# Kernel tuning notes

Hardware: AMD Instinct MI355X
Metric: run time of the kernel (lower is better)

## Reference

```python
import jax, jax.numpy as jnp
import numpy as np
from jax import lax

DIM = 256
NUM_HEADS = 8
HEAD_DIM = DIM // NUM_HEADS
SCALE = HEAD_DIM ** -0.5


def _avg_pool(x, k, p):
    # torch AvgPool2d(kernel=k, stride=1, padding=p) with count_include_pad=True
    s = lax.reduce_window(x, 0.0, lax.add,
                          window_dimensions=(1, 1, k, k),
                          window_strides=(1, 1, 1, 1),
                          padding=((0, 0), (0, 0), (p, p), (p, p)))
    return s / (k * k)


def setup_inputs() -> dict:
    key = jax.random.key(0)
    ks = jax.random.split(key, 7)
    x = jax.random.normal(ks[0], (2, DIM, 48, 48), dtype=jnp.float32)
    q_w = jax.random.normal(ks[1], (DIM, DIM), dtype=jnp.float32) * (DIM ** -0.5)
    q_b = jax.random.normal(ks[2], (DIM,), dtype=jnp.float32) * 0.02
    kv_w = jax.random.normal(ks[3], (2 * DIM, DIM), dtype=jnp.float32) * (DIM ** -0.5)
    kv_b = jax.random.normal(ks[4], (2 * DIM,), dtype=jnp.float32) * 0.02
    proj_w = jax.random.normal(ks[5], (DIM, DIM), dtype=jnp.float32) * (DIM ** -0.5)
    proj_b = jax.random.normal(ks[6], (DIM,), dtype=jnp.float32) * 0.02
    return {"x": x, "q_w": q_w, "q_b": q_b, "kv_w": kv_w, "kv_b": kv_b,
            "proj_w": proj_w, "proj_b": proj_b}


def reference(x, q_w, q_b, kv_w, kv_b, proj_w, proj_b):
    B, C, H, W = x.shape
    h, d, N = NUM_HEADS, HEAD_DIM, H * W

    # q = 1x1 conv -> [B, h, N, d]
    q = jnp.einsum('oc,bchw->bohw', q_w, x) + q_b[None, :, None, None]
    q = q.reshape(B, h, d, N).transpose(0, 1, 3, 2)

    # kv is a linear 1x1 conv, so (kv(x)+kv(p1)+kv(p2)+kv(p3))/4 == kv(mean of inputs)
    x_avg = (x + _avg_pool(x, 3, 1) + _avg_pool(x, 5, 2) + _avg_pool(x, 7, 3)) / 4.0
    kv = jnp.einsum('oc,bchw->bohw', kv_w, x_avg) + kv_b[None, :, None, None]
    kv = kv.reshape(B, 2, h, d, N).transpose(1, 0, 2, 4, 3)  # [2, B, h, N, d]
    k, v = kv[0], kv[1]

    attn = jnp.einsum('bhnd,bhmd->bhnm', q, k) * SCALE  # [B, h, N, N]
    attn = jax.nn.softmax(attn, axis=-1)
    y = jnp.einsum('bhnm,bhmd->bhnd', attn, v)  # [B, h, N, d]
    # faithful to torch: transpose(1,2) then flat reshape to [B, C, H, W]
    y = y.transpose(0, 2, 1, 3).reshape(B, C, H, W)

    out = jnp.einsum('oc,bchw->bohw', proj_w, y) + proj_b[None, :, None, None]
    return out
```

## Files before the change

kernel.cpp:

```cpp
#include <hip/hip_runtime.h>
#include <hip/hip_bf16.h>
#include <cstdint>

#define DIMC  256
#define NH    8
#define HD    32
#define NPIX  2304
#define BATCH 2
#define NSPLIT 6
#define KPS   384
#define KT    32
#define NT    (KPS / KT)

typedef short s16x8 __attribute__((ext_vector_type(8)));
typedef short s16x4 __attribute__((ext_vector_type(4)));
typedef float f32x4 __attribute__((ext_vector_type(4)));

#define MFMA32(A,B,C) __builtin_amdgcn_mfma_f32_16x16x32_bf16(A,B,C,0,0,0)

__device__ inline uint32_t rnau(float x) { return __float_as_uint(x) + 0x8000u; }
__device__ inline uint32_t pk2(uint32_t l_, uint32_t h_) {
  return __builtin_amdgcn_perm(h_, l_, 0x07060302u);
}

__global__ __launch_bounds__(256) void pool_kernel(const float* __restrict__ x,
                                                   float* __restrict__ xavg) {
  const int plane = blockIdx.x;
  const float* xp = x + (size_t)plane * NPIX;
  __shared__ float sx[NPIX];
  __shared__ float h3[NPIX], h5[NPIX], h7[NPIX];
  const int t = threadIdx.x;
#pragma unroll
  for (int r = 0; r < 9; ++r) sx[r * 256 + t] = xp[r * 256 + t];
  __syncthreads();
#pragma unroll
  for (int r = 0; r < 9; ++r) {
    int p = r * 256 + t;
    int i = p / 48, j = p - i * 48;
    float a3 = 0.f, a5 = 0.f, a7 = 0.f;
#pragma unroll
    for (int dj = -3; dj <= 3; ++dj) {
      int jj = j + dj;
      if (jj < 0 || jj >= 48) continue;
      float v = sx[i * 48 + jj];
      a7 += v;
      if (dj >= -2 && dj <= 2) a5 += v;
      if (dj >= -1 && dj <= 1) a3 += v;
    }
    h3[p] = a3; h5[p] = a5; h7[p] = a7;
  }
  __syncthreads();
#pragma unroll
  for (int r = 0; r < 9; ++r) {
    int p = r * 256 + t;
    int i = p / 48, j = p - i * 48;
    float b3 = 0.f, b5 = 0.f, b7 = 0.f;
#pragma unroll
    for (int di = -3; di <= 3; ++di) {
      int ii = i + di;
      if (ii < 0 || ii >= 48) continue;
      int q = ii * 48 + j;
      b7 += h7[q];
      if (di >= -2 && di <= 2) b5 += h5[q];
      if (di >= -1 && di <= 1) b3 += h3[q];
    }
    xavg[(size_t)plane * NPIX + p] =
        0.25f * (sx[p] + b3 * (1.f / 9.f) + b5 * (1.f / 25.f) + b7 * (1.f / 49.f));
  }
}

__global__ __launch_bounds__(256) void conv_all(
    const float* __restrict__ x, const float* __restrict__ xavg,
    const float* __restrict__ qw, const float* __restrict__ kvw,
    const float* __restrict__ pw_,
    short* __restrict__ Xh, short* __restrict__ Ah,
    short* __restrict__ Wth) {
  const int bx = blockIdx.x;
  const int t = threadIdx.x;
  if (bx < 576) {
    const float* src = (bx < 288) ? x : xavg;
    short* dhi = (bx < 288) ? Xh : Ah;
    const int bb = (bx < 288) ? bx : bx - 288;
    const int n0 = (bb % 36) * 64, c0 = ((bb / 36) & 3) * 64, b = bb / 144;
    __shared__ __align__(16) float T[64][68];
    {
      const int c = t >> 2, n4 = (t & 3) * 16;
      const float* sp = src + ((size_t)b * DIMC + c0 + c) * NPIX + n0 + n4;
#pragma unroll
      for (int i2 = 0; i2 < 4; ++i2)
        *(f32x4*)&T[c][n4 + i2 * 4] = *(const f32x4*)(sp + i2 * 4);
    }
    __syncthreads();
    {
      const int n = t >> 2, c4 = (t & 3) * 16;
      float v[16];
#pragma unroll
      for (int i = 0; i < 16; ++i) v[i] = T[c4 + i][n];
      uint32_t a[16];
#pragma unroll
      for (int i = 0; i < 16; ++i) a[i] = rnau(v[i]);
      union { s16x8 s; uint32_t u[4]; } H0, H1;
#pragma unroll
      for (int j = 0; j < 4; ++j) {
        H0.u[j] = pk2(a[2 * j], a[2 * j + 1]);
        H1.u[j] = pk2(a[8 + 2 * j], a[8 + 2 * j + 1]);
      }
      const size_t off = ((size_t)b * NPIX + n0 + n) * DIMC + c0 + c4;
      *(s16x8*)(dhi + off) = H0.s; *(s16x8*)(dhi + off + 8) = H1.s;
    }
  } else {
    const int idx = ((bx - 576) * 256 + t) * 8;
    const float* s;
    int off;
    if (idx < 65536)       { s = qw;  off = idx; }
    else if (idx < 196608) { s = kvw; off = idx - 65536; }
    else                   { s = pw_; off = idx - 196608; }
    f32x4 x0 = *(const f32x4*)(s + off);
    f32x4 x1 = *(const f32x4*)(s + off + 4);
    float v[8] = {x0[0], x0[1], x0[2], x0[3], x1[0], x1[1], x1[2], x1[3]};
    uint32_t a[8];
#pragma unroll
    for (int i = 0; i < 8; ++i) a[i] = rnau(v[i]);
    union { s16x8 s; uint32_t u[4]; } H;
#pragma unroll
    for (int j = 0; j < 4; ++j) H.u[j] = pk2(a[2 * j], a[2 * j + 1]);
    *(s16x8*)(Wth + idx) = H.s;
  }
}

__global__ __launch_bounds__(128) void gemm_qkv_hi(
    const short* __restrict__ Wth,
    const float* __restrict__ q_b, const float* __restrict__ kv_b,
    const short* __restrict__ Xh, const short* __restrict__ Ah,
    short* __restrict__ Qhi, short* __restrict__ Khi, short* __restrict__ Vhi,
    float qscale) {
  __shared__ __align__(16) float Cl[32][68];
  const int by = blockIdx.y;
  const bool isQ = (by < 8);
  const int o0 = isQ ? by * 32 : (by - 8) * 32;
  const short* Wh = isQ ? Wth : Wth + 65536;
  const float* bias = isQ ? q_b : kv_b;
  const short* Inh = isQ ? Xh : Ah;
  const float scale = isQ ? qscale : 1.0f;
  short* d1 = isQ ? Qhi : Khi;
  const int n0 = blockIdx.x * 64;
  const int b  = blockIdx.z;

  const int tid = threadIdx.x;
  const int wave = tid >> 6, lane = tid & 63;
  const int g = lane >> 4, q = lane & 15;

  const short* wph = Wh + ((o0 + wave * 16 + q) * DIMC + g * 8);
  const short* iph = Inh + ((size_t)(b * NPIX + n0 + q) * DIMC + g * 8);

  f32x4 acc[4] = {{0,0,0,0},{0,0,0,0},{0,0,0,0},{0,0,0,0}};
#pragma unroll
  for (int c0 = 0; c0 < DIMC; c0 += 32) {
    s16x8 ah = *(const s16x8*)(wph + c0);
#pragma unroll
    for (int st = 0; st < 4; ++st) {
      s16x8 bh_ = *(const s16x8*)(iph + (size_t)st * 16 * DIMC + c0);
      acc[st] = MFMA32(ah, bh_, acc[st]);
    }
  }
#pragma unroll
  for (int st = 0; st < 4; ++st)
#pragma unroll
    for (int r = 0; r < 4; ++r)
      Cl[wave * 16 + g * 4 + r][st * 16 + q] = acc[st][r];
  __syncthreads();

  if (o0 < 256) {
    const int n = tid >> 1, oq = tid & 1;
    const int h = o0 >> 5;
    const float* bp = bias + o0 + oq * 16;
    float v[16];
#pragma unroll
    for (int i = 0; i < 16; ++i) v[i] = (Cl[oq * 16 + i][n] + bp[i]) * scale;
    uint32_t a[16];
#pragma unroll
    for (int i = 0; i < 16; ++i) a[i] = rnau(v[i]);
    union { s16x8 s; uint32_t u[4]; } H0, H1;
#pragma unroll
    for (int j = 0; j < 4; ++j) {
      H0.u[j] = pk2(a[2 * j], a[2 * j + 1]);
      H1.u[j] = pk2(a[8 + 2 * j], a[8 + 2 * j + 1]);
    }
    const size_t off = ((size_t)((b * 8 + h) * NPIX + n0 + n)) * HD + oq * 16;
    *(s16x8*)(d1 + off) = H0.s; *(s16x8*)(d1 + off + 8) = H1.s;
  } else {
    const int o = tid >> 2, nc = (tid & 3) * 16;
    const int h = (o0 - 256) >> 5;
    const float bv = bias[o0 + o];
    float v[16];
#pragma unroll
    for (int i2 = 0; i2 < 4; ++i2) {
      f32x4 t4 = *(const f32x4*)&Cl[o][nc + i2 * 4];
      v[i2 * 4 + 0] = t4[0] + bv; v[i2 * 4 + 1] = t4[1] + bv;
      v[i2 * 4 + 2] = t4[2] + bv; v[i2 * 4 + 3] = t4[3] + bv;
    }
    uint32_t a[16];
#pragma unroll
    for (int i = 0; i < 16; ++i) a[i] = rnau(v[i]);
    union { s16x8 s; uint32_t u[4]; } H0, H1;
#pragma unroll
    for (int j = 0; j < 4; ++j) {
      H0.u[j] = pk2(a[2 * j], a[2 * j + 1]);
      H1.u[j] = pk2(a[8 + 2 * j], a[8 + 2 * j + 1]);
    }
    const size_t off = ((size_t)((b * 8 + h) * HD + o)) * NPIX + n0 + nc;
    *(s16x8*)(Vhi + off) = H0.s; *(s16x8*)(Vhi + off + 8) = H1.s;
  }
}

__global__ __launch_bounds__(128) void attn_mfma(
    const short* __restrict__ Qhi,
    const short* __restrict__ Khi,
    const short* __restrict__ Vhi,
    short* __restrict__ part_o,
    float* __restrict__ part_l) {
  const int sb = blockIdx.x;
  const int bh = sb / 36;
  const int qb = sb % 36;
  const int split = blockIdx.y;
  const int tid = threadIdx.x;
  const int wave = tid >> 6, lane = tid & 63;
  const int g = lane >> 4, q = lane & 15;
  const int base = qb * 64 + wave * 32;

  __shared__ __align__(16) short Plds[2][2][16 * 40];
  short* pwA = &Plds[wave][0][0];
  short* pwB = &Plds[wave][1][0];

  const size_t qoff = ((size_t)bh * NPIX + base + q) * HD + g * 8;
  const s16x8 qhA = *(const s16x8*)(Qhi + qoff);
  const s16x8 qhB = *(const s16x8*)(Qhi + qoff + 16 * HD);

  const short* kp = Khi + ((size_t)bh * NPIX + split * KPS + q) * HD + g * 8;
  const short* vp = Vhi + ((size_t)bh * HD + q) * NPIX + split * KPS + g * 8;

  const f32x4 Z4 = {0.f, 0.f, 0.f, 0.f};
  f32x4 OA0 = Z4, OA1 = Z4, OB0 = Z4, OB1 = Z4;
  f32x4 LA = Z4, LB = Z4;
  s16x8 kb[3][2], vb[3][2], pfA, pfB, vp0, vp1;

  union { s16x8 s; uint32_t u[4]; } ONE;
  ONE.u[0] = 0x3F803F80u; ONE.u[1] = 0x3F803F80u;
  ONE.u[2] = 0x3F803F80u; ONE.u[3] = 0x3F803F80u;
  const s16x8 ones = ONE.s;

  kb[0][0] = *(const s16x8*)(kp);
  kb[0][1] = *(const s16x8*)(kp + 16 * HD);
  vb[0][0] = *(const s16x8*)(vp);
  vb[0][1] = *(const s16x8*)(vp + 16 * NPIX);
  kb[1][0] = *(const s16x8*)(kp + KT * HD);
  kb[1][1] = *(const s16x8*)(kp + KT * HD + 16 * HD);
  vb[1][0] = *(const s16x8*)(vp + KT);
  vb[1][1] = *(const s16x8*)(vp + KT + 16 * NPIX);

#pragma unroll
  for (int t = 0; t < NT; ++t) {
    const int cur = t % 3;
    if (t + 2 < NT) {
      const int nx2 = (t + 2) % 3;
      const short* kpn = kp + (t + 2) * (KT * HD);
      const short* vpn = vp + (t + 2) * KT;
      kb[nx2][0] = *(const s16x8*)(kpn);
      kb[nx2][1] = *(const s16x8*)(kpn + 16 * HD);
      vb[nx2][0] = *(const s16x8*)(vpn);
      vb[nx2][1] = *(const s16x8*)(vpn + 16 * NPIX);
    }
    f32x4 SA0 = MFMA32(kb[cur][0], qhA, Z4);
    f32x4 SA1 = MFMA32(kb[cur][1], qhA, Z4);
    f32x4 SB0 = MFMA32(kb[cur][0], qhB, Z4);
    f32x4 SB1 = MFMA32(kb[cur][1], qhB, Z4);
    if (t > 0) {
      OA0 = MFMA32(vp0, pfA, OA0);
      OA1 = MFMA32(vp1, pfA, OA1);
      OB0 = MFMA32(vp0, pfB, OB0);
      OB1 = MFMA32(vp1, pfB, OB1);
      LA  = MFMA32(ones, pfA, LA);
      LB  = MFMA32(ones, pfB, LB);
    }
    {
      f32x4 p0, p1;
#pragma unroll
      for (int r = 0; r < 4; ++r) { p0[r] = exp2f(SA0[r]); p1[r] = exp2f(SA1[r]); }
      uint2 w0, w1;
      w0.x = pk2(rnau(p0[0]), rnau(p0[1])); w0.y = pk2(rnau(p0[2]), rnau(p0[3]));
      w1.x = pk2(rnau(p1[0]), rnau(p1[1])); w1.y = pk2(rnau(p1[2]), rnau(p1[3]));
      *(uint2*)&pwA[q * 40 + g * 4] = w0;
      *(uint2*)&pwA[q * 40 + 16 + g * 4] = w1;
    }
    {
      f32x4 p0, p1;
#pragma unroll
      for (int r = 0; r < 4; ++r) { p0[r] = exp2f(SB0[r]); p1[r] = exp2f(SB1[r]); }
      uint2 w0, w1;
      w0.x = pk2(rnau(p0[0]), rnau(p0[1])); w0.y = pk2(rnau(p0[2]), rnau(p0[3]));
      w1.x = pk2(rnau(p1[0]), rnau(p1[1])); w1.y = pk2(rnau(p1[2]), rnau(p1[3]));
      *(uint2*)&pwB[q * 40 + g * 4] = w0;
      *(uint2*)&pwB[q * 40 + 16 + g * 4] = w1;
    }
    vp0 = vb[cur][0]; vp1 = vb[cur][1];
    pfA = *(const s16x8*)&pwA[q * 40 + g * 8];
    pfB = *(const s16x8*)&pwB[q * 40 + g * 8];
  }
  OA0 = MFMA32(vp0, pfA, OA0);
  OA1 = MFMA32(vp1, pfA, OA1);
  OB0 = MFMA32(vp0, pfB, OB0);
  OB1 = MFMA32(vp1, pfB, OB1);
  LA  = MFMA32(ones, pfA, LA);
  LB  = MFMA32(ones, pfB, LB);

  const int rowA = bh * NPIX + base + q;
  const int rowB = rowA + 16;
  short* poA = part_o + ((size_t)rowA * NSPLIT + split) * HD;
  short* poB = part_o + ((size_t)rowB * NSPLIT + split) * HD;
  uint2 wa0, wa1, wb0, wb1;
  wa0.x = pk2(rnau(OA0[0]), rnau(OA0[1])); wa0.y = pk2(rnau(OA0[2]), rnau(OA0[3]));
  wa1.x = pk2(rnau(OA1[0]), rnau(OA1[1])); wa1.y = pk2(rnau(OA1[2]), rnau(OA1[3]));
  wb0.x = pk2(rnau(OB0[0]), rnau(OB0[1])); wb0.y = pk2(rnau(OB0[2]), rnau(OB0[3]));
  wb1.x = pk2(rnau(OB1[0]), rnau(OB1[1])); wb1.y = pk2(rnau(OB1[2]), rnau(OB1[3]));
  *(uint2*)(poA + g * 4)      = wa0;
  *(uint2*)(poA + 16 + g * 4) = wa1;
  *(uint2*)(poB + g * 4)      = wb0;
  *(uint2*)(poB + 16 + g * 4) = wb1;
  if (g == 0) {
    part_l[(size_t)rowA * NSPLIT + split] = LA[0];
    part_l[(size_t)rowB * NSPLIT + split] = LB[0];
  }
}

__global__ __launch_bounds__(256) void proj_fused(
    const short* __restrict__ Wh,
    const float* __restrict__ bias,
    const short* __restrict__ part_o,
    const float* __restrict__ part_l,
    float* __restrict__ out) {
  const int n0 = blockIdx.x * 64;
  const int o0 = blockIdx.y * 64;
  const int b  = blockIdx.z;
  const int r9 = n0 >> 8;
  const int h0 = (n0 & 255) >> 5;
  const int tid = threadIdx.x;

  __shared__ __align__(16) short Zt[64][272];
  __shared__ float Li[256][2];
  __shared__ __align__(16) float Cl[64][68];

  for (int e = tid; e < 512; e += 256) {
    const int c = e >> 1, hh = e & 1;
    const float* pl = part_l +
        ((size_t)(b * 8 + h0 + hh) * NPIX + 9 * c + r9) * NSPLIT;
    Li[c][hh] = 1.f / (pl[0] + pl[1] + pl[2] + pl[3] + pl[4] + pl[5]);
  }
  __syncthreads();

  {
    const int dd = tid & 63, qq = tid >> 6;
    const int hh = dd >> 5, d = dd & 31;
    const short* pob = part_o +
        ((size_t)(b * 8 + h0 + hh) * NPIX) * (NSPLIT * HD) + d;
#pragma unroll
    for (int cg = 0; cg < 8; ++cg) {
      const int cb = qq * 64 + cg * 8;
      uint32_t a[8];
#pragma unroll
      for (int j = 0; j < 8; ++j) {
        const int c = cb + j;
        const short* po = pob + (size_t)(9 * c + r9) * (NSPLIT * HD);
        float acc = 0.f;
#pragma unroll
        for (int s = 0; s < NSPLIT; ++s)
          acc += __uint_as_float(((uint32_t)(unsigned short)po[s * HD]) << 16);
        a[j] = rnau(acc * Li[c][hh]);
      }
      union { s16x8 s; uint32_t u[4]; } H;
#pragma unroll
      for (int j2 = 0; j2 < 4; ++j2) H.u[j2] = pk2(a[2 * j2], a[2 * j2 + 1]);
      *(s16x8*)&Zt[dd][cb] = H.s;
    }
  }
  __syncthreads();

  const int wave = tid >> 6, lane = tid & 63;
  const int g = lane >> 4, q = lane & 15;
  const short* wph = Wh + ((o0 + wave * 16 + q) * DIMC + g * 8);
  f32x4 acc[4] = {{0,0,0,0},{0,0,0,0},{0,0,0,0},{0,0,0,0}};
#pragma unroll
  for (int c0 = 0; c0 < DIMC; c0 += 32) {
    s16x8 ah = *(const s16x8*)(wph + c0);
#pragma unroll
    for (int st = 0; st < 4; ++st) {
      s16x8 bh_ = *(const s16x8*)&Zt[st * 16 + q][c0 + g * 8];
      acc[st] = MFMA32(ah, bh_, acc[st]);
    }
  }
#pragma unroll
  for (int st = 0; st < 4; ++st)
#pragma unroll
    for (int r = 0; r < 4; ++r)
      Cl[wave * 16 + g * 4 + r][st * 16 + q] = acc[st][r];
  __syncthreads();

  const int o = tid >> 2, nc = (tid & 3) * 16;
  const float bv = bias[o0 + o];
  float* op = out + ((size_t)b * DIMC + o0 + o) * NPIX + n0 + nc;
#pragma unroll
  for (int i2 = 0; i2 < 4; ++i2) {
    f32x4 v = *(const f32x4*)&Cl[o][nc + i2 * 4];
    v[0] += bv; v[1] += bv; v[2] += bv; v[3] += bv;
    *(f32x4*)(op + i2 * 4) = v;
  }
}

extern "C" void kernel_launch(void* const* d_in, const int* in_sizes, int n_in,
                              void* d_out, int out_size, void* d_ws, size_t ws_size,
                              hipStream_t stream) {
  const float* x      = (const float*)d_in[0];
  const float* q_w    = (const float*)d_in[1];
  const float* q_b    = (const float*)d_in[2];
  const float* kv_w   = (const float*)d_in[3];
  const float* kv_b   = (const float*)d_in[4];
  const float* proj_w = (const float*)d_in[5];
  const float* proj_b = (const float*)d_in[6];
  float* out = (float*)d_out;

  char* w = (char*)d_ws;
  float* xavg = (float*)w;
  short* Xh   = (short*)(w + 4718592);
  short* Ah   = (short*)(w + 9437184);
  short* part_o = (short*)w;
  short* Wth  = (short*)(w + 28311552);
  short* Qhi  = (short*)(w + 29360128);
  short* Khi  = (short*)(w + 31719424);
  short* Vhi  = (short*)(w + 34078720);
  float* part_l = (float*)(w + 36438016);

  const float qscale = 0.17677669529663689f * 1.4426950408889634f;

  pool_kernel<<<BATCH * DIMC, 256, 0, stream>>>(x, xavg);
  conv_all<<<704, 256, 0, stream>>>(x, xavg, q_w, kv_w, proj_w, Xh, Ah, Wth);
  gemm_qkv_hi<<<dim3(36, 24, 2), 128, 0, stream>>>(Wth, q_b, kv_b,
                                                   Xh, Ah, Qhi, Khi, Vhi, qscale);
  attn_mfma<<<dim3(16 * 36, NSPLIT), 128, 0, stream>>>(Qhi, Khi, Vhi, part_o, part_l);
  proj_fused<<<dim3(36, 4, 2), 256, 0, stream>>>(Wth + 196608, proj_b,
                                                 part_o, part_l, out);
}
```

Measured before the change: 150.1 us.

## Drop KV split in attention, normalize in-kernel, write transposed Z for simple proj GEMM

Removes the 6-way split over keys so each attention block walks all 2304 keys, normalizes by the row sum itself, and scatters bf16 output straight into a [B, N, C] layout matching the torch transpose/reshape. The projection kernel then becomes a plain GEMM reading Z from global memory, with no partial reduction or LDS staging. This removes the partial-output round trip and the merge work, but cuts attention grid parallelism sixfold (576 blocks of 2 waves) and uses scattered 2-byte stores.

After: 165.6 us. 10.4% more time.

```diff
diff --git a/kernel.cpp b/kernel.cpp
--- a/kernel.cpp
+++ b/kernel.cpp
@@ -7,10 +7,8 @@
 #define HD    32
 #define NPIX  2304
 #define BATCH 2
-#define NSPLIT 6
-#define KPS   384
 #define KT    32
-#define NT    (KPS / KT)
+#define NT2   (NPIX / KT)
 
 typedef short s16x8 __attribute__((ext_vector_type(8)));
 typedef short s16x4 __attribute__((ext_vector_type(4)));
@@ -217,12 +215,10 @@
     const short* __restrict__ Qhi,
     const short* __restrict__ Khi,
     const short* __restrict__ Vhi,
-    short* __restrict__ part_o,
-    float* __restrict__ part_l) {
+    short* __restrict__ zh) {
   const int sb = blockIdx.x;
   const int bh = sb / 36;
   const int qb = sb % 36;
-  const int split = blockIdx.y;
   const int tid = threadIdx.x;
   const int wave = tid >> 6, lane = tid & 63;
   const int g = lane >> 4, q = lane & 15;
@@ -236,18 +232,21 @@
   const s16x8 qhA = *(const s16x8*)(Qhi + qoff);
   const s16x8 qhB = *(const s16x8*)(Qhi + qoff + 16 * HD);
 
-  const short* kp = Khi + ((size_t)bh * NPIX + split * KPS + q) * HD + g * 8;
-  const short* vp = Vhi + ((size_t)bh * HD + q) * NPIX + split * KPS + g * 8;
+  const short* kp = Khi + ((size_t)bh * NPIX + q) * HD + g * 8;
+  const short* vp = Vhi + ((size_t)bh * HD + q) * NPIX + g * 8;
 
   const f32x4 Z4 = {0.f, 0.f, 0.f, 0.f};
   f32x4 OA0 = Z4, OA1 = Z4, OB0 = Z4, OB1 = Z4;
   f32x4 LA = Z4, LB = Z4;
   s16x8 kb[3][2], vb[3][2], pfA, pfB, vp0, vp1;
 
-  union { s16x8 s; uint32_t u[4]; } ONE;
+  union { s16x8 s; uint32_t u[4]; } ONE, ZZ;
   ONE.u[0] = 0x3F803F80u; ONE.u[1] = 0x3F803F80u;
   ONE.u[2] = 0x3F803F80u; ONE.u[3] = 0x3F803F80u;
+  ZZ.u[0] = 0; ZZ.u[1] = 0; ZZ.u[2] = 0; ZZ.u[3] = 0;
   const s16x8 ones = ONE.s;
+  pfA = ZZ.s; pfB = ZZ.s;
+  vp0 = ones; vp1 = ones;
 
   kb[0][0] = *(const s16x8*)(kp);
   kb[0][1] = *(const s16x8*)(kp + 16 * HD);
@@ -258,54 +257,63 @@
   vb[1][0] = *(const s16x8*)(vp + KT);
   vb[1][1] = *(const s16x8*)(vp + KT + 16 * NPIX);
 
-#pragma unroll
-  for (int t = 0; t < NT; ++t) {
-    const int cur = t % 3;
-    if (t + 2 < NT) {
-      const int nx2 = (t + 2) % 3;
-      const short* kpn = kp + (t + 2) * (KT * HD);
-      const short* vpn = vp + (t + 2) * KT;
-      kb[nx2][0] = *(const s16x8*)(kpn);
-      kb[nx2][1] = *(const s16x8*)(kpn + 16 * HD);
-      vb[nx2][0] = *(const s16x8*)(vpn);
-      vb[nx2][1] = *(const s16x8*)(vpn + 16 * NPIX);
-    }
-    f32x4 SA0 = MFMA32(kb[cur][0], qhA, Z4);
-    f32x4 SA1 = MFMA32(kb[cur][1], qhA, Z4);
-    f32x4 SB0 = MFMA32(kb[cur][0], qhB, Z4);
-    f32x4 SB1 = MFMA32(kb[cur][1], qhB, Z4);
-    if (t > 0) {
-      OA0 = MFMA32(vp0, pfA, OA0);
-      OA1 = MFMA32(vp1, pfA, OA1);
-      OB0 = MFMA32(vp0, pfB, OB0);
-      OB1 = MFMA32(vp1, pfB, OB1);
-      LA  = MFMA32(ones, pfA, LA);
-      LB  = MFMA32(ones, pfB, LB);
-    }
-    {
-      f32x4 p0, p1;
-#pragma unroll
-      for (int r = 0; r < 4; ++r) { p0[r] = exp2f(SA0[r]); p1[r] = exp2f(SA1[r]); }
-      uint2 w0, w1;
-      w0.x = pk2(rnau(p0[0]), rnau(p0[1])); w0.y = pk2(rnau(p0[2]), rnau(p0[3]));
-      w1.x = pk2(rnau(p1[0]), rnau(p1[1])); w1.y = pk2(rnau(p1[2]), rnau(p1[3]));
-      *(uint2*)&pwA[q * 40 + g * 4] = w0;
-      *(uint2*)&pwA[q * 40 + 16 + g * 4] = w1;
-    }
-    {
-      f32x4 p0, p1;
-#pragma unroll
-      for (int r = 0; r < 4; ++r) { p0[r] = exp2f(SB0[r]); p1[r] = exp2f(SB1[r]); }
-      uint2 w0, w1;
-      w0.x = pk2(rnau(p0[0]), rnau(p0[1])); w0.y = pk2(rnau(p0[2]), rnau(p0[3]));
-      w1.x = pk2(rnau(p1[0]), rnau(p1[1])); w1.y = pk2(rnau(p1[2]), rnau(p1[3]));
-      *(uint2*)&pwB[q * 40 + g * 4] = w0;
-      *(uint2*)&pwB[q * 40 + 16 + g * 4] = w1;
-    }
-    vp0 = vb[cur][0]; vp1 = vb[cur][1];
-    pfA = *(const s16x8*)&pwA[q * 40 + g * 8];
-    pfB = *(const s16x8*)&pwB[q * 40 + g * 8];
-  }
+#define ATTN_STEP(CUR, NX2, T)                                                \
+  {                                                                           \
+    if ((T) + 2 < NT2) {                                                      \
+      const short* kpn = kp + ((T) + 2) * (KT * HD);                          \
+      const short* vpn = vp + ((T) + 2) * KT;                                 \
+      kb[NX2][0] = *(const s16x8*)(kpn);                                      \
+      kb[NX2][1] = *(const s16x8*)(kpn + 16 * HD);                            \
+      vb[NX2][0] = *(const s16x8*)(vpn);                                      \
+      vb[NX2][1] = *(const s16x8*)(vpn + 16 * NPIX);                          \
+    }                                                                         \
+    f32x4 SA0 = MFMA32(kb[CUR][0], qhA, Z4);                                  \
+    f32x4 SA1 = MFMA32(kb[CUR][1], qhA, Z4);                                  \
+    f32x4 SB0 = MFMA32(kb[CUR][0], qhB, Z4);                                  \
+    f32x4 SB1 = MFMA32(kb[CUR][1], qhB, Z4);                                  \
+    OA0 = MFMA32(vp0, pfA, OA0);                                              \
+    OA1 = MFMA32(vp1, pfA, OA1);                                              \
+    OB0 = MFMA32(vp0, pfB, OB0);                                              \
+    OB1 = MFMA32(vp1, pfB, OB1);                                              \
+    LA  = MFMA32(ones, pfA, LA);                                              \
+    LB  = MFMA32(ones, pfB, LB);                                              \
+    {                                                                         \
+      f32x4 p0, p1;                                                           \
+      p0[0] = exp2f(SA0[0]); p0[1] = exp2f(SA0[1]);                           \
+      p0[2] = exp2f(SA0[2]); p0[3] = exp2f(SA0[3]);                           \
+      p1[0] = exp2f(SA1[0]); p1[1] = exp2f(SA1[1]);                           \
+      p1[2] = exp2f(SA1[2]); p1[3] = exp2f(SA1[3]);                           \
+      uint2 w0, w1;                                                           \
+      w0.x = pk2(rnau(p0[0]), rnau(p0[1])); w0.y = pk2(rnau(p0[2]), rnau(p0[3])); \
+      w1.x = pk2(rnau(p1[0]), rnau(p1[1])); w1.y = pk2(rnau(p1[2]), rnau(p1[3])); \
+      *(uint2*)&pwA[q * 40 + g * 4] = w0;                                     \
+      *(uint2*)&pwA[q * 40 + 16 + g * 4] = w1;                                \
+    }                                                                         \
+    {                                                                         \
+      f32x4 p0, p1;                                                           \
+      p0[0] = exp2f(SB0[0]); p0[1] = exp2f(SB0[1]);                           \
+      p0[2] = exp2f(SB0[2]); p0[3] = exp2f(SB0[3]);                           \
+      p1[0] = exp2f(SB1[0]); p1[1] = exp2f(SB1[1]);                           \
+      p1[2] = exp2f(SB1[2]); p1[3] = exp2f(SB1[3]);                           \
+      uint2 w0, w1;                                                           \
+      w0.x = pk2(rnau(p0[0]), rnau(p0[1])); w0.y = pk2(rnau(p0[2]), rnau(p0[3])); \
+      w1.x = pk2(rnau(p1[0]), rnau(p1[1])); w1.y = pk2(rnau(p1[2]), rnau(p1[3])); \
+      *(uint2*)&pwB[q * 40 + g * 4] = w0;                                     \
+      *(uint2*)&pwB[q * 40 + 16 + g * 4] = w1;                                \
+    }                                                                         \
+    vp0 = vb[CUR][0]; vp1 = vb[CUR][1];                                       \
+    pfA = *(const s16x8*)&pwA[q * 40 + g * 8];                                \
+    pfB = *(const s16x8*)&pwB[q * 40 + g * 8];                                \
+  }
+
+#pragma unroll 1
+  for (int tt = 0; tt < NT2; tt += 3) {
+    ATTN_STEP(0, 2, tt);
+    ATTN_STEP(1, 0, tt + 1);
+    ATTN_STEP(2, 1, tt + 2);
+  }
+#undef ATTN_STEP
+
   OA0 = MFMA32(vp0, pfA, OA0);
   OA1 = MFMA32(vp1, pfA, OA1);
   OB0 = MFMA32(vp0, pfB, OB0);
@@ -313,87 +321,53 @@
   LA  = MFMA32(ones, pfA, LA);
   LB  = MFMA32(ones, pfB, LB);
 
-  const int rowA = bh * NPIX + base + q;
-  const int rowB = rowA + 16;
-  short* poA = part_o + ((size_t)rowA * NSPLIT + split) * HD;
-  short* poB = part_o + ((size_t)rowB * NSPLIT + split) * HD;
-  uint2 wa0, wa1, wb0, wb1;
-  wa0.x = pk2(rnau(OA0[0]), rnau(OA0[1])); wa0.y = pk2(rnau(OA0[2]), rnau(OA0[3]));
-  wa1.x = pk2(rnau(OA1[0]), rnau(OA1[1])); wa1.y = pk2(rnau(OA1[2]), rnau(OA1[3]));
-  wb0.x = pk2(rnau(OB0[0]), rnau(OB0[1])); wb0.y = pk2(rnau(OB0[2]), rnau(OB0[3]));
-  wb1.x = pk2(rnau(OB1[0]), rnau(OB1[1])); wb1.y = pk2(rnau(OB1[2]), rnau(OB1[3]));
-  *(uint2*)(poA + g * 4)      = wa0;
-  *(uint2*)(poA + 16 + g * 4) = wa1;
-  *(uint2*)(poB + g * 4)      = wb0;
-  *(uint2*)(poB + 16 + g * 4) = wb1;
-  if (g == 0) {
-    part_l[(size_t)rowA * NSPLIT + split] = LA[0];
-    part_l[(size_t)rowB * NSPLIT + split] = LB[0];
-  }
-}
-
-__global__ __launch_bounds__(256) void proj_fused(
+  const float invA = 1.f / LA[0];
+  const float invB = 1.f / LB[0];
+  const int h = bh & 7, b = bh >> 3;
+  const int nA = base + q, nB = nA + 16;
+  {
+    const int cA = nA / 9, rA = nA - cA * 9;
+    short* zp = zh + ((size_t)(b * NPIX + rA * 256 + h * HD)) * DIMC + cA;
+#pragma unroll
+    for (int rr = 0; rr < 4; ++rr) {
+      zp[(size_t)(g * 4 + rr) * DIMC]      = (short)(rnau(OA0[rr] * invA) >> 16);
+      zp[(size_t)(16 + g * 4 + rr) * DIMC] = (short)(rnau(OA1[rr] * invA) >> 16);
+    }
+  }
+  {
+    const int cB = nB / 9, rB = nB - cB * 9;
+    short* zp = zh + ((size_t)(b * NPIX + rB * 256 + h * HD)) * DIMC + cB;
+#pragma unroll
+    for (int rr = 0; rr < 4; ++rr) {
+      zp[(size_t)(g * 4 + rr) * DIMC]      = (short)(rnau(OB0[rr] * invB) >> 16);
+      zp[(size_t)(16 + g * 4 + rr) * DIMC] = (short)(rnau(OB1[rr] * invB) >> 16);
+    }
+  }
+}
+
+__global__ __launch_bounds__(128) void gemm_proj_hi(
     const short* __restrict__ Wh,
     const float* __restrict__ bias,
-    const short* __restrict__ part_o,
-    const float* __restrict__ part_l,
+    const short* __restrict__ Zh,
     float* __restrict__ out) {
+  __shared__ __align__(16) float Cl[32][68];
   const int n0 = blockIdx.x * 64;
-  const int o0 = blockIdx.y * 64;
+  const int o0 = blockIdx.y * 32;
   const int b  = blockIdx.z;
-  const int r9 = n0 >> 8;
-  const int h0 = (n0 & 255) >> 5;
   const int tid = threadIdx.x;
-
-  __shared__ __align__(16) short Zt[64][272];
-  __shared__ float Li[256][2];
-  __shared__ __align__(16) float Cl[64][68];
-
-  for (int e = tid; e < 512; e += 256) {
-    const int c = e >> 1, hh = e & 1;
-    const float* pl = part_l +
-        ((size_t)(b * 8 + h0 + hh) * NPIX + 9 * c + r9) * NSPLIT;
-    Li[c][hh] = 1.f / (pl[0] + pl[1] + pl[2] + pl[3] + pl[4] + pl[5]);
-  }
-  __syncthreads();
-
-  {
-    const int dd = tid & 63, qq = tid >> 6;
-    const int hh = dd >> 5, d = dd & 31;
-    const short* pob = part_o +
-        ((size_t)(b * 8 + h0 + hh) * NPIX) * (NSPLIT * HD) + d;
-#pragma unroll
-    for (int cg = 0; cg < 8; ++cg) {
-      const int cb = qq * 64 + cg * 8;
-      uint32_t a[8];
-#pragma unroll
-      for (int j = 0; j < 8; ++j) {
-        const int c = cb + j;
-        const short* po = pob + (size_t)(9 * c + r9) * (NSPLIT * HD);
-        float acc = 0.f;
-#pragma unroll
-        for (int s = 0; s < NSPLIT; ++s)
-          acc += __uint_as_float(((uint32_t)(unsigned short)po[s * HD]) << 16);
-        a[j] = rnau(acc * Li[c][hh]);
-      }
-      union { s16x8 s; uint32_t u[4]; } H;
-#pragma unroll
-      for (int j2 = 0; j2 < 4; ++j2) H.u[j2] = pk2(a[2 * j2], a[2 * j2 + 1]);
-      *(s16x8*)&Zt[dd][cb] = H.s;
-    }
-  }
-  __syncthreads();
-
   const int wave = tid >> 6, lane = tid & 63;
   const int g = lane >> 4, q = lane & 15;
+
   const short* wph = Wh + ((o0 + wave * 16 + q) * DIMC + g * 8);
+  const short* iph = Zh + ((size_t)(b * NPIX + n0 + q) * DIMC + g * 8);
+
   f32x4 acc[4] = {{0,0,0,0},{0,0,0,0},{0,0,0,0},{0,0,0,0}};
 #pragma unroll
   for (int c0 = 0; c0 < DIMC; c0 += 32) {
     s16x8 ah = *(const s16x8*)(wph + c0);
 #pragma unroll
     for (int st = 0; st < 4; ++st) {
-      s16x8 bh_ = *(const s16x8*)&Zt[st * 16 + q][c0 + g * 8];
+      s16x8 bh_ = *(const s16x8*)(iph + (size_t)st * 16 * DIMC + c0);
       acc[st] = MFMA32(ah, bh_, acc[st]);
     }
   }
@@ -431,12 +405,11 @@
   float* xavg = (float*)w;
   short* Xh   = (short*)(w + 4718592);
   short* Ah   = (short*)(w + 9437184);
-  short* part_o = (short*)w;
   short* Wth  = (short*)(w + 28311552);
   short* Qhi  = (short*)(w + 29360128);
   short* Khi  = (short*)(w + 31719424);
   short* Vhi  = (short*)(w + 34078720);
-  float* part_l = (float*)(w + 36438016);
+  short* Zh   = (short*)(w + 37322752);
 
   const float qscale = 0.17677669529663689f * 1.4426950408889634f;
 
@@ -444,7 +417,6 @@
   conv_all<<<704, 256, 0, stream>>>(x, xavg, q_w, kv_w, proj_w, Xh, Ah, Wth);
   gemm_qkv_hi<<<dim3(36, 24, 2), 128, 0, stream>>>(Wth, q_b, kv_b,
                                                    Xh, Ah, Qhi, Khi, Vhi, qscale);
-  attn_mfma<<<dim3(16 * 36, NSPLIT), 128, 0, stream>>>(Qhi, Khi, Vhi, part_o, part_l);
-  proj_fused<<<dim3(36, 4, 2), 256, 0, stream>>>(Wth + 196608, proj_b,
-                                                 part_o, part_l, out);
-}
+  attn_mfma<<<576, 128, 0, stream>>>(Qhi, Khi, Vhi, Zh);
+  gemm_proj_hi<<<dim3(36, 8, 2), 128, 0, stream>>>(Wth + 196608, proj_b, Zh, out);
+}
```
